# Performance work log

Measured on AMD Instinct MI355X. Metric: run time of the kernel, lower is better.

The kernel has to match this reference:

```python
import jax, jax.numpy as jnp
import numpy as np

INIT_RANGE = 0.02

def setup_inputs() -> dict:
    key = jax.random.key(0)
    ks = jax.random.split(key, 5)
    B, S, D, H, Dh = 4, 2048, 768, 12, 64
    residual = jax.random.normal(ks[0], (B, S, D), dtype=jnp.float32)
    W_Q = jax.random.normal(ks[1], (H, D, Dh), dtype=jnp.float32) * INIT_RANGE
    W_K = jax.random.normal(ks[2], (H, D, Dh), dtype=jnp.float32) * INIT_RANGE
    W_V = jax.random.normal(ks[3], (H, D, Dh), dtype=jnp.float32) * INIT_RANGE
    W_O = jax.random.normal(ks[4], (H, Dh, D), dtype=jnp.float32) * INIT_RANGE
    b_Q = jnp.zeros((H, Dh), dtype=jnp.float32)
    b_K = jnp.zeros((H, Dh), dtype=jnp.float32)
    b_V = jnp.zeros((H, Dh), dtype=jnp.float32)
    b_O = jnp.zeros((D,), dtype=jnp.float32)
    return {"residual": residual, "W_Q": W_Q, "W_K": W_K, "W_V": W_V,
            "W_O": W_O, "b_Q": b_Q, "b_K": b_K, "b_V": b_V, "b_O": b_O}

def reference(residual, W_Q, W_K, W_V, W_O, b_Q, b_K, b_V, b_O):
    # residual: [b, s, d]; W_{Q,K,V}: [h, d, dh]; W_O: [h, dh, d]
    d_head = W_Q.shape[-1]
    q = jnp.einsum('bsd,hde->bshe', residual, W_Q) + b_Q  # [b, s, h, dh]
    k = jnp.einsum('bsd,hde->bshe', residual, W_K) + b_K
    v = jnp.einsum('bsd,hde->bshe', residual, W_V) + b_V
    scores = jnp.einsum('bqhe,bkhe->bhqk', q, k) / jnp.sqrt(jnp.float32(d_head))
    S = residual.shape[1]
    causal = jnp.tril(jnp.ones((S, S), dtype=bool))  # True where attending allowed
    scores = jnp.where(causal, scores, -jnp.inf)
    pattern = jax.nn.softmax(scores, axis=-1)  # [b, h, q, k]
    z = jnp.einsum('bkhe,bhqk->bqhe', v, pattern)  # [b, q, h, dh]
    attn_out = jnp.einsum('bqhe,hed->bqd', z, W_O) + b_O
    return attn_out
```

## Files before the change

### kernel.cpp

```cpp
#include <hip/hip_runtime.h>

typedef short short8 __attribute__((ext_vector_type(8)));
typedef float floatx4 __attribute__((ext_vector_type(4)));
typedef unsigned short ushort_t;


__device__ inline ushort_t f2bf(float f) {
  union { float f; unsigned u; } x; x.f = f;
  unsigned u = x.u;
  unsigned r = u + 0x7fffu + ((u >> 16) & 1u);
  return (ushort_t)(r >> 16);
}

__device__ inline unsigned pk2(float a, float b) {
  union { float f; unsigned u; } x, y; x.f = a; y.f = b;
  return ((x.u + 0x8000u) >> 16) | ((y.u + 0x8000u) & 0xffff0000u);
}

__device__ inline float fexp2(float x) {
#if __has_builtin(__builtin_amdgcn_exp2f)
  return __builtin_amdgcn_exp2f(x);
#else
  return exp2f(x);
#endif
}

__device__ inline void async16(const void* g, void* l) {
  __builtin_amdgcn_global_load_lds((const __attribute__((address_space(1))) void*)g,
                                   (__attribute__((address_space(3))) void*)l,
                                   16, 0, 0);
}


__global__ __launch_bounds__(256) void conv_rx(const float* __restrict__ x,
                                               ushort_t* __restrict__ y, int n4) {
  int i = blockIdx.x * 256 + threadIdx.x;
  if (i >= n4) return;
  float4 f = ((const float4*)x)[i];
  ushort4 o;
  o.x = f2bf(f.x); o.y = f2bf(f.y); o.z = f2bf(f.z); o.w = f2bf(f.w);
  ((ushort4*)y)[i] = o;
}

__global__ __launch_bounds__(256) void conv_w(
    const float* __restrict__ wq, const float* __restrict__ wk, const float* __restrict__ wv,
    const float* __restrict__ wo,
    const float* __restrict__ bq, const float* __restrict__ bk, const float* __restrict__ bv,
    ushort_t* __restrict__ wqkvT, ushort_t* __restrict__ woT, float* __restrict__ bqkv)
{
  int i = blockIdx.x * 256 + threadIdx.x;
  const int NQKV = 2304 * 768;
  const int NO = 768 * 768;
  if (i < NQKV) {
    int c = i / 768, d = i - c * 768;
    int m = c / 768, rem = c - m * 768;
    int h = rem >> 6, e = rem & 63;
    const float* w = (m == 0) ? wq : ((m == 1) ? wk : wv);
    wqkvT[i] = f2bf(w[(h * 768 + d) * 64 + e]);
  } else if (i < NQKV + NO) {
    int j = i - NQKV;
    int dd = j / 768, he = j - dd * 768;
    woT[j] = f2bf(wo[he * 768 + dd]);
  } else if (i < NQKV + NO + 2304) {
    int c = i - NQKV - NO;
    int m = c / 768, rem = c - m * 768;
    const float* bp = (m == 0) ? bq : ((m == 1) ? bk : bv);
    bqkv[c] = bp[rem];
  }
}


__global__ __launch_bounds__(256) void gemm128(
    const ushort_t* __restrict__ A, const ushort_t* __restrict__ Bt,
    const float* __restrict__ bias, int mode,
    ushort_t* __restrict__ q, ushort_t* __restrict__ k, ushort_t* __restrict__ v,
    float* __restrict__ outf)
{
  __shared__ ushort_t lA[128 * 32];
  __shared__ ushort_t lB[128 * 32];
  const int tid = threadIdx.x;
  const int wave = tid >> 6, lane = tid & 63;
  const int ln15 = lane & 15, quad = lane >> 4;
  const int row0 = blockIdx.x * 128, col0 = blockIdx.y * 128;
  const int wm = (wave >> 1) * 64, wn = (wave & 1) * 64;
  const int c0 = wave * 2;

  const ushort_t* gA0 = A + (size_t)(row0 + c0 * 16 + (lane >> 2)) * 768 + (lane & 3) * 8;
  const ushort_t* gB0 = Bt + (size_t)(col0 + c0 * 16 + (lane >> 2)) * 768 + (lane & 3) * 8;

  floatx4 acc[4][4];
#pragma unroll
  for (int mi = 0; mi < 4; ++mi)
#pragma unroll
    for (int ni = 0; ni < 4; ++ni)
      acc[mi][ni] = (floatx4){0.f, 0.f, 0.f, 0.f};

  for (int kt = 0; kt < 24; ++kt) {
    __syncthreads();
    async16(gA0 + kt * 32, &lA[c0 * 512]);
    async16(gA0 + kt * 32 + 16 * 768, &lA[c0 * 512 + 512]);
    async16(gB0 + kt * 32, &lB[c0 * 512]);
    async16(gB0 + kt * 32 + 16 * 768, &lB[c0 * 512 + 512]);
    __syncthreads();
    short8 af[4], bfv[4];
#pragma unroll
    for (int mi = 0; mi < 4; ++mi)
      af[mi] = *(const short8*)&lA[(wm + mi * 16 + ln15) * 32 + quad * 8];
#pragma unroll
    for (int ni = 0; ni < 4; ++ni)
      bfv[ni] = *(const short8*)&lB[(wn + ni * 16 + ln15) * 32 + quad * 8];
#pragma unroll
    for (int mi = 0; mi < 4; ++mi)
#pragma unroll
      for (int ni = 0; ni < 4; ++ni)
        acc[mi][ni] = __builtin_amdgcn_mfma_f32_16x16x32_bf16(af[mi], bfv[ni], acc[mi][ni], 0, 0, 0);
  }

  const float qscale = 0.125f * 1.44269504f;
#pragma unroll
  for (int mi = 0; mi < 4; ++mi) {
#pragma unroll
    for (int ni = 0; ni < 4; ++ni) {
      int gr = row0 + wm + mi * 16 + quad * 4;
      int gc = col0 + wn + ni * 16 + ln15;
      float bia = bias[gc];
#pragma unroll
      for (int r = 0; r < 4; ++r) {
        float val = acc[mi][ni][r] + bia;
        int rr = gr + r;
        if (mode == 0) {
          int m = gc / 768;
          int rem = gc - m * 768;
          int h = rem >> 6, e = rem & 63;
          int bb = rr >> 11, ss = rr & 2047;
          size_t dst = ((size_t)((bb * 12 + h) * 2048 + ss) << 6) + e;
          ushort_t* dp = (m == 0) ? q : ((m == 1) ? k : v);
          dp[dst] = f2bf((m == 0) ? val * qscale : val);
        } else {
          outf[(size_t)rr * 768 + gc] = val;
        }
      }
    }
  }
}


__global__ __launch_bounds__(256) void transpose_v(const ushort_t* __restrict__ v,
                                                   ushort_t* __restrict__ vt)
{
  __shared__ ushort_t t[64 * 72];
  const int bh = blockIdx.y;
  const int s0 = blockIdx.x * 64;
  const ushort_t* src = v + ((size_t)bh * 2048 + s0) * 64;
#pragma unroll
  for (int t2 = 0; t2 < 2; ++t2) {
    int task = t2 * 256 + threadIdx.x;
    int row = task >> 3, ch = task & 7;
    short8 d = *(const short8*)(src + row * 64 + ch * 8);
    *(short8*)&t[row * 72 + ch * 8] = d;
  }
  __syncthreads();
  ushort_t* dst = vt + (size_t)bh * 64 * 2048 + s0;
#pragma unroll
  for (int t2 = 0; t2 < 2; ++t2) {
    int task = t2 * 256 + threadIdx.x;
    int e = task >> 3, sc = task & 7;
    short8 d;
#pragma unroll
    for (int j = 0; j < 8; ++j)
      d[j] = (short)t[(sc * 8 + j) * 72 + e];
    *(short8*)(dst + (size_t)e * 2048 + sc * 8) = d;
  }
}


__device__ inline short8 frag_ld(const ushort_t* t, int row, int ch) {
  return *(const short8*)&t[row * 64 + (((ch ^ row) & 7) * 8)];
}

__global__ __launch_bounds__(256) void attn3(
    const ushort_t* __restrict__ Q, const ushort_t* __restrict__ K,
    const ushort_t* __restrict__ VT, ushort_t* __restrict__ Z)
{
  __shared__ ushort_t lK[2][64 * 64];
  __shared__ ushort_t lV[2][64 * 64];
  __shared__ ushort_t lPQ[128 * 64];
  const int tid = threadIdx.x;
  const int wave = tid >> 6, lane = tid & 63;
  const int ln15 = lane & 15, quad = lane >> 4;
  const int bi = blockIdx.x;
  const int bh = bi % 48;
  const int t = 15 - (bi / 48);
  const int h = bh % 12, b = bh / 12;
  const size_t base = (size_t)bh * 2048 * 64;
  const ushort_t* Qp = Q + base + (size_t)t * 128 * 64;
  const ushort_t* Kp = K + base;
  const ushort_t* Vp = VT + base;
  const int nk = 2 * t + 2;

#pragma unroll
  for (int i = 0; i < 4; ++i) {
    int task = i * 256 + tid;
    int row = task >> 3, lch = task & 7;
    int c = lch ^ (row & 7);
    async16(Qp + row * 64 + c * 8, &lPQ[task * 8]);
  }
#pragma unroll
  for (int i = 0; i < 2; ++i) {
    int task = i * 256 + tid;
    int row = task >> 3, lch = task & 7;
    int c = lch ^ (row & 7);
    async16(Kp + (size_t)row * 64 + c * 8, &lK[0][task * 8]);
    async16(Vp + (size_t)row * 2048 + c * 8, &lV[0][task * 8]);
  }
  __syncthreads();
  short8 qf[2][2];
#pragma unroll
  for (int c = 0; c < 2; ++c) {
    qf[c][0] = frag_ld(lPQ, wave * 32 + c * 16 + ln15, quad);
    qf[c][1] = frag_ld(lPQ, wave * 32 + c * 16 + ln15, quad + 4);
  }
  __syncthreads();

  float l_i[2] = {0.f, 0.f};
  floatx4 o[2][4];
#pragma unroll
  for (int c = 0; c < 2; ++c)
#pragma unroll
    for (int et = 0; et < 4; ++et) o[c][et] = (floatx4){0.f, 0.f, 0.f, 0.f};

  ushort_t* lPw = lPQ + wave * 2048;
  const int qg0 = t * 128 + wave * 32 + ln15;

  for (int kt = 0; kt < nk; ++kt) {
    const int buf = kt & 1;
    if (kt + 1 < nk) {
#pragma unroll
      for (int i = 0; i < 2; ++i) {
        int task = i * 256 + tid;
        int row = task >> 3, lch = task & 7;
        int c = lch ^ (row & 7);
        async16(Kp + (size_t)((kt + 1) * 64 + row) * 64 + c * 8, &lK[buf ^ 1][task * 8]);
        async16(Vp + (size_t)row * 2048 + (kt + 1) * 64 + c * 8, &lV[buf ^ 1][task * 8]);
      }
    }

    floatx4 st[2][4];
#pragma unroll
    for (int ni = 0; ni < 4; ++ni) {
      short8 kf0 = frag_ld(lK[buf], ni * 16 + ln15, quad);
      short8 kf1 = frag_ld(lK[buf], ni * 16 + ln15, quad + 4);
#pragma unroll
      for (int c = 0; c < 2; ++c) {
        floatx4 z4 = (floatx4){0.f, 0.f, 0.f, 0.f};
        z4 = __builtin_amdgcn_mfma_f32_16x16x32_bf16(kf0, qf[c][0], z4, 0, 0, 0);
        st[c][ni] = __builtin_amdgcn_mfma_f32_16x16x32_bf16(kf1, qf[c][1], z4, 0, 0, 0);
      }
    }

    const bool masked = (kt >= 2 * t);
#pragma unroll
    for (int c = 0; c < 2; ++c) {
      const int qg = qg0 + c * 16;
      float p[16];
      float rs = 0.f;
#pragma unroll
      for (int ni = 0; ni < 4; ++ni)
#pragma unroll
        for (int r = 0; r < 4; ++r) {
          float x = st[c][ni][r];
          if (masked) {
            int kg = kt * 64 + ni * 16 + quad * 4 + r;
            x = (kg <= qg) ? x : -1e30f;
          }
          float pe = fexp2(x);
          p[ni * 4 + r] = pe;
          rs += pe;
        }
      rs += __shfl_xor(rs, 16);
      rs += __shfl_xor(rs, 32);
      l_i[c] += rs;
      const int rowl = c * 16 + ln15;
#pragma unroll
      for (int ni = 0; ni < 4; ++ni) {
        int chunk = 2 * ni + (quad >> 1);
        int pos = chunk ^ (rowl & 7);
        uint2 w;
        w.x = pk2(p[ni * 4 + 0], p[ni * 4 + 1]);
        w.y = pk2(p[ni * 4 + 2], p[ni * 4 + 3]);
        *(uint2*)&lPw[rowl * 64 + pos * 8 + (quad & 1) * 4] = w;
      }
    }

    short8 pf[2][2];
#pragma unroll
    for (int c = 0; c < 2; ++c) {
      pf[c][0] = frag_ld(lPw, c * 16 + ln15, quad);
      pf[c][1] = frag_ld(lPw, c * 16 + ln15, quad + 4);
    }
#pragma unroll
    for (int et = 0; et < 4; ++et) {
      short8 vf0 = frag_ld(lV[buf], et * 16 + ln15, quad);
      short8 vf1 = frag_ld(lV[buf], et * 16 + ln15, quad + 4);
#pragma unroll
      for (int c = 0; c < 2; ++c) {
        o[c][et] = __builtin_amdgcn_mfma_f32_16x16x32_bf16(vf0, pf[c][0], o[c][et], 0, 0, 0);
        o[c][et] = __builtin_amdgcn_mfma_f32_16x16x32_bf16(vf1, pf[c][1], o[c][et], 0, 0, 0);
      }
    }
    __syncthreads();
  }

#pragma unroll
  for (int c = 0; c < 2; ++c) {
    float inv = 1.f / l_i[c];
    size_t zrow = (size_t)(b * 2048 + t * 128 + wave * 32 + c * 16 + ln15);
#pragma unroll
    for (int et = 0; et < 4; ++et) {
      ushort4 w;
      w.x = f2bf(o[c][et][0] * inv);
      w.y = f2bf(o[c][et][1] * inv);
      w.z = f2bf(o[c][et][2] * inv);
      w.w = f2bf(o[c][et][3] * inv);
      *(ushort4*)&Z[zrow * 768 + h * 64 + et * 16 + quad * 4] = w;
    }
  }
}


extern "C" void kernel_launch(void* const* d_in, const int* in_sizes, int n_in,
                              void* d_out, int out_size, void* d_ws, size_t ws_size,
                              hipStream_t stream)
{
  const float* residual = (const float*)d_in[0];
  const float* W_Q = (const float*)d_in[1];
  const float* W_K = (const float*)d_in[2];
  const float* W_V = (const float*)d_in[3];
  const float* W_O = (const float*)d_in[4];
  const float* b_Q = (const float*)d_in[5];
  const float* b_K = (const float*)d_in[6];
  const float* b_V = (const float*)d_in[7];
  const float* b_O = (const float*)d_in[8];
  float* out = (float*)d_out;

  char* w = (char*)d_ws;
  ushort_t* rx    = (ushort_t*)(w + 0);
  ushort_t* wqkvT = (ushort_t*)(w + 12582912);
  ushort_t* woT   = (ushort_t*)(w + 16121856);
  float*    bqkv  = (float*)   (w + 17301504);
  ushort_t* q     = (ushort_t*)(w + 17310720);
  ushort_t* k     = (ushort_t*)(w + 29893632);
  ushort_t* v     = (ushort_t*)(w + 42476544);
  ushort_t* vt    = (ushort_t*)(w + 55059456);
  ushort_t* z     = rx;

  conv_rx<<<6144, 256, 0, stream>>>(residual, rx, 8192 * 768 / 4);
  conv_w<<<(2304 * 768 + 768 * 768 + 2304 + 255) / 256, 256, 0, stream>>>(
      W_Q, W_K, W_V, W_O, b_Q, b_K, b_V, wqkvT, woT, bqkv);
  gemm128<<<dim3(64, 18), 256, 0, stream>>>(rx, wqkvT, bqkv, 0, q, k, v, nullptr);
  transpose_v<<<dim3(32, 48), 256, 0, stream>>>(v, vt);
  attn3<<<768, 256, 0, stream>>>(q, k, vt, z);
  gemm128<<<dim3(64, 6), 256, 0, stream>>>(z, woT, b_O, 1, nullptr, nullptr, nullptr, out);
}
```

Measured before the change: 231.1 us.

## Double-buffer GEMM LDS loads, tile weight conversion, split out-projection GEMM

Rewrites the weight conversion kernel as an LDS-tiled transpose, so global reads and writes are coalesced instead of strided per element. Both GEMMs now double-buffer their LDS tiles, issuing the next k-tile's async loads before computing on the current one, which removes one barrier per iteration. The output projection gets its own kernel with 64-row tiles, doubling the block count to improve occupancy across CUs. This adds LDS usage and raises the chance of load/compute ordering hazards around the single barrier.

```diff
diff --git a/kernel.cpp b/kernel.cpp
--- a/kernel.cpp
+++ b/kernel.cpp
@@ -42,42 +42,83 @@
   ((ushort4*)y)[i] = o;
 }
 
-__global__ __launch_bounds__(256) void conv_w(
+__global__ __launch_bounds__(256) void conv_w2(
     const float* __restrict__ wq, const float* __restrict__ wk, const float* __restrict__ wv,
     const float* __restrict__ wo,
     const float* __restrict__ bq, const float* __restrict__ bk, const float* __restrict__ bv,
     ushort_t* __restrict__ wqkvT, ushort_t* __restrict__ woT, float* __restrict__ bqkv)
 {
-  int i = blockIdx.x * 256 + threadIdx.x;
-  const int NQKV = 2304 * 768;
-  const int NO = 768 * 768;
-  if (i < NQKV) {
-    int c = i / 768, d = i - c * 768;
-    int m = c / 768, rem = c - m * 768;
-    int h = rem >> 6, e = rem & 63;
+  __shared__ ushort_t t[64 * 72];
+  const int bid = blockIdx.x;
+  const int tid = threadIdx.x;
+  if (bid < 432) {
+    int m = bid / 144, rem = bid % 144;
+    int h = rem / 12, dt = rem % 12;
+    int d0 = dt * 64;
     const float* w = (m == 0) ? wq : ((m == 1) ? wk : wv);
-    wqkvT[i] = f2bf(w[(h * 768 + d) * 64 + e]);
-  } else if (i < NQKV + NO) {
-    int j = i - NQKV;
-    int dd = j / 768, he = j - dd * 768;
-    woT[j] = f2bf(wo[he * 768 + dd]);
-  } else if (i < NQKV + NO + 2304) {
-    int c = i - NQKV - NO;
-    int m = c / 768, rem = c - m * 768;
-    const float* bp = (m == 0) ? bq : ((m == 1) ? bk : bv);
-    bqkv[c] = bp[rem];
-  }
-}
-
-
-__global__ __launch_bounds__(256) void gemm128(
+    const float* src = w + ((size_t)h * 768 + d0) * 64;
+#pragma unroll
+    for (int i = 0; i < 4; ++i) {
+      int task = i * 256 + tid;
+      int row = task >> 4, c4 = task & 15;
+      float4 f = *(const float4*)(src + row * 64 + c4 * 4);
+      ushort4 o4;
+      o4.x = f2bf(f.x); o4.y = f2bf(f.y); o4.z = f2bf(f.z); o4.w = f2bf(f.w);
+      *(ushort4*)&t[row * 72 + c4 * 4] = o4;
+    }
+    __syncthreads();
+    ushort_t* dst = wqkvT + ((size_t)m * 768 + h * 64) * 768 + d0;
+#pragma unroll
+    for (int i = 0; i < 2; ++i) {
+      int task = i * 256 + tid;
+      int e = task >> 3, sc = task & 7;
+      short8 d8;
+#pragma unroll
+      for (int j = 0; j < 8; ++j) d8[j] = (short)t[(sc * 8 + j) * 72 + e];
+      *(short8*)(dst + (size_t)e * 768 + sc * 8) = d8;
+    }
+  } else if (bid < 576) {
+    int b2 = bid - 432;
+    int het = b2 / 12, dt = b2 % 12;
+    int he0 = het * 64, d0 = dt * 64;
+    const float* src = wo + (size_t)he0 * 768 + d0;
+#pragma unroll
+    for (int i = 0; i < 4; ++i) {
+      int task = i * 256 + tid;
+      int row = task >> 4, c4 = task & 15;
+      float4 f = *(const float4*)(src + (size_t)row * 768 + c4 * 4);
+      ushort4 o4;
+      o4.x = f2bf(f.x); o4.y = f2bf(f.y); o4.z = f2bf(f.z); o4.w = f2bf(f.w);
+      *(ushort4*)&t[row * 72 + c4 * 4] = o4;
+    }
+    __syncthreads();
+    ushort_t* dst = woT + (size_t)d0 * 768 + he0;
+#pragma unroll
+    for (int i = 0; i < 2; ++i) {
+      int task = i * 256 + tid;
+      int dd = task >> 3, sc = task & 7;
+      short8 d8;
+#pragma unroll
+      for (int j = 0; j < 8; ++j) d8[j] = (short)t[(sc * 8 + j) * 72 + dd];
+      *(short8*)(dst + (size_t)dd * 768 + sc * 8) = d8;
+    }
+  } else {
+    for (int idx = tid; idx < 2304; idx += 256) {
+      int m = idx / 768, rem = idx - m * 768;
+      const float* bp = (m == 0) ? bq : ((m == 1) ? bk : bv);
+      bqkv[idx] = bp[rem];
+    }
+  }
+}
+
+
+__global__ __launch_bounds__(256) void gemm_qkv(
     const ushort_t* __restrict__ A, const ushort_t* __restrict__ Bt,
-    const float* __restrict__ bias, int mode,
-    ushort_t* __restrict__ q, ushort_t* __restrict__ k, ushort_t* __restrict__ v,
-    float* __restrict__ outf)
-{
-  __shared__ ushort_t lA[128 * 32];
-  __shared__ ushort_t lB[128 * 32];
+    const float* __restrict__ bias,
+    ushort_t* __restrict__ q, ushort_t* __restrict__ k, ushort_t* __restrict__ v)
+{
+  __shared__ ushort_t lA[2][128 * 32];
+  __shared__ ushort_t lB[2][128 * 32];
   const int tid = threadIdx.x;
   const int wave = tid >> 6, lane = tid & 63;
   const int ln15 = lane & 15, quad = lane >> 4;
@@ -95,25 +136,33 @@
     for (int ni = 0; ni < 4; ++ni)
       acc[mi][ni] = (floatx4){0.f, 0.f, 0.f, 0.f};
 
+  async16(gA0, &lA[0][c0 * 512]);
+  async16(gA0 + 16 * 768, &lA[0][c0 * 512 + 512]);
+  async16(gB0, &lB[0][c0 * 512]);
+  async16(gB0 + 16 * 768, &lB[0][c0 * 512 + 512]);
+  __syncthreads();
+
   for (int kt = 0; kt < 24; ++kt) {
-    __syncthreads();
-    async16(gA0 + kt * 32, &lA[c0 * 512]);
-    async16(gA0 + kt * 32 + 16 * 768, &lA[c0 * 512 + 512]);
-    async16(gB0 + kt * 32, &lB[c0 * 512]);
-    async16(gB0 + kt * 32 + 16 * 768, &lB[c0 * 512 + 512]);
-    __syncthreads();
+    const int buf = kt & 1;
+    if (kt + 1 < 24) {
+      async16(gA0 + (kt + 1) * 32, &lA[buf ^ 1][c0 * 512]);
+      async16(gA0 + (kt + 1) * 32 + 16 * 768, &lA[buf ^ 1][c0 * 512 + 512]);
+      async16(gB0 + (kt + 1) * 32, &lB[buf ^ 1][c0 * 512]);
+      async16(gB0 + (kt + 1) * 32 + 16 * 768, &lB[buf ^ 1][c0 * 512 + 512]);
+    }
     short8 af[4], bfv[4];
 #pragma unroll
     for (int mi = 0; mi < 4; ++mi)
-      af[mi] = *(const short8*)&lA[(wm + mi * 16 + ln15) * 32 + quad * 8];
+      af[mi] = *(const short8*)&lA[buf][(wm + mi * 16 + ln15) * 32 + quad * 8];
 #pragma unroll
     for (int ni = 0; ni < 4; ++ni)
-      bfv[ni] = *(const short8*)&lB[(wn + ni * 16 + ln15) * 32 + quad * 8];
+      bfv[ni] = *(const short8*)&lB[buf][(wn + ni * 16 + ln15) * 32 + quad * 8];
 #pragma unroll
     for (int mi = 0; mi < 4; ++mi)
 #pragma unroll
       for (int ni = 0; ni < 4; ++ni)
         acc[mi][ni] = __builtin_amdgcn_mfma_f32_16x16x32_bf16(af[mi], bfv[ni], acc[mi][ni], 0, 0, 0);
+    __syncthreads();
   }
 
   const float qscale = 0.125f * 1.44269504f;
@@ -124,22 +173,83 @@
       int gr = row0 + wm + mi * 16 + quad * 4;
       int gc = col0 + wn + ni * 16 + ln15;
       float bia = bias[gc];
+      int m = gc / 768;
+      int rem = gc - m * 768;
+      int h = rem >> 6, e = rem & 63;
+      ushort_t* dp = (m == 0) ? q : ((m == 1) ? k : v);
 #pragma unroll
       for (int r = 0; r < 4; ++r) {
         float val = acc[mi][ni][r] + bia;
         int rr = gr + r;
-        if (mode == 0) {
-          int m = gc / 768;
-          int rem = gc - m * 768;
-          int h = rem >> 6, e = rem & 63;
-          int bb = rr >> 11, ss = rr & 2047;
-          size_t dst = ((size_t)((bb * 12 + h) * 2048 + ss) << 6) + e;
-          ushort_t* dp = (m == 0) ? q : ((m == 1) ? k : v);
-          dp[dst] = f2bf((m == 0) ? val * qscale : val);
-        } else {
-          outf[(size_t)rr * 768 + gc] = val;
-        }
+        int bb = rr >> 11, ss = rr & 2047;
+        size_t dst = ((size_t)((bb * 12 + h) * 2048 + ss) << 6) + e;
+        dp[dst] = f2bf((m == 0) ? val * qscale : val);
       }
+    }
+  }
+}
+
+
+__global__ __launch_bounds__(256) void gemm_out(
+    const ushort_t* __restrict__ A, const ushort_t* __restrict__ Bt,
+    const float* __restrict__ bias, float* __restrict__ outf)
+{
+  __shared__ ushort_t lA[2][64 * 32];
+  __shared__ ushort_t lB[2][128 * 32];
+  const int tid = threadIdx.x;
+  const int wave = tid >> 6, lane = tid & 63;
+  const int ln15 = lane & 15, quad = lane >> 4;
+  const int row0 = blockIdx.x * 64, col0 = blockIdx.y * 128;
+  const int wm = (wave >> 1) * 32, wn = (wave & 1) * 64;
+  const int cb = wave * 2;
+
+  const ushort_t* gA0 = A + (size_t)(row0 + wave * 16 + (lane >> 2)) * 768 + (lane & 3) * 8;
+  const ushort_t* gB0 = Bt + (size_t)(col0 + cb * 16 + (lane >> 2)) * 768 + (lane & 3) * 8;
+
+  floatx4 acc[2][4];
+#pragma unroll
+  for (int mi = 0; mi < 2; ++mi)
+#pragma unroll
+    for (int ni = 0; ni < 4; ++ni)
+      acc[mi][ni] = (floatx4){0.f, 0.f, 0.f, 0.f};
+
+  async16(gA0, &lA[0][wave * 512]);
+  async16(gB0, &lB[0][cb * 512]);
+  async16(gB0 + 16 * 768, &lB[0][cb * 512 + 512]);
+  __syncthreads();
+
+  for (int kt = 0; kt < 24; ++kt) {
+    const int buf = kt & 1;
+    if (kt + 1 < 24) {
+      async16(gA0 + (kt + 1) * 32, &lA[buf ^ 1][wave * 512]);
+      async16(gB0 + (kt + 1) * 32, &lB[buf ^ 1][cb * 512]);
+      async16(gB0 + (kt + 1) * 32 + 16 * 768, &lB[buf ^ 1][cb * 512 + 512]);
+    }
+    short8 af[2], bfv[4];
+#pragma unroll
+    for (int mi = 0; mi < 2; ++mi)
+      af[mi] = *(const short8*)&lA[buf][(wm + mi * 16 + ln15) * 32 + quad * 8];
+#pragma unroll
+    for (int ni = 0; ni < 4; ++ni)
+      bfv[ni] = *(const short8*)&lB[buf][(wn + ni * 16 + ln15) * 32 + quad * 8];
+#pragma unroll
+    for (int mi = 0; mi < 2; ++mi)
+#pragma unroll
+      for (int ni = 0; ni < 4; ++ni)
+        acc[mi][ni] = __builtin_amdgcn_mfma_f32_16x16x32_bf16(af[mi], bfv[ni], acc[mi][ni], 0, 0, 0);
+    __syncthreads();
+  }
+
+#pragma unroll
+  for (int mi = 0; mi < 2; ++mi) {
+#pragma unroll
+    for (int ni = 0; ni < 4; ++ni) {
+      int gr = row0 + wm + mi * 16 + quad * 4;
+      int gc = col0 + wn + ni * 16 + ln15;
+      float bia = bias[gc];
+#pragma unroll
+      for (int r = 0; r < 4; ++r)
+        outf[(size_t)(gr + r) * 768 + gc] = acc[mi][ni][r] + bia;
     }
   }
 }
@@ -355,10 +465,9 @@
   ushort_t* z     = rx;
 
   conv_rx<<<6144, 256, 0, stream>>>(residual, rx, 8192 * 768 / 4);
-  conv_w<<<(2304 * 768 + 768 * 768 + 2304 + 255) / 256, 256, 0, stream>>>(
-      W_Q, W_K, W_V, W_O, b_Q, b_K, b_V, wqkvT, woT, bqkv);
-  gemm128<<<dim3(64, 18), 256, 0, stream>>>(rx, wqkvT, bqkv, 0, q, k, v, nullptr);
+  conv_w2<<<577, 256, 0, stream>>>(W_Q, W_K, W_V, W_O, b_Q, b_K, b_V, wqkvT, woT, bqkv);
+  gemm_qkv<<<dim3(64, 18), 256, 0, stream>>>(rx, wqkvT, bqkv, q, k, v);
   transpose_v<<<dim3(32, 48), 256, 0, stream>>>(v, vt);
   attn3<<<768, 256, 0, stream>>>(q, k, vt, z);
-  gemm128<<<dim3(64, 6), 256, 0, stream>>>(z, woT, b_O, 1, nullptr, nullptr, nullptr, out);
-}
+  gemm_out<<<dim3(128, 6), 256, 0, stream>>>(z, woT, b_O, out);
+}
```

New measurement: 230.5 us. No clear change (-0.2%).
